# Kernel tuning notes

Hardware: AMD Instinct MI355X
Metric: run time of the kernel (lower is better)

Reference implementation:

```python
import jax, jax.numpy as jnp
import numpy as np

T, B, IN, H, OUT = 512, 1024, 128, 256, 4

def setup_inputs() -> dict:
    key = jax.random.key(0)
    ks = jax.random.split(key, 6)
    return {
        "inp": jax.random.normal(ks[0], (T, B, IN), dtype=jnp.float32),
        "hidden": jnp.zeros((B, H), dtype=jnp.float32),
        "W_i2h": jax.random.normal(ks[1], (H, IN + H), dtype=jnp.float32) * (1.0 / np.sqrt(IN + H)),
        "b_i2h": jax.random.normal(ks[2], (H,), dtype=jnp.float32) * 0.01,
        "W_i2o": jax.random.normal(ks[3], (OUT, IN + H), dtype=jnp.float32) * (1.0 / np.sqrt(IN + H)),
        "b_i2o": jax.random.normal(ks[4], (OUT,), dtype=jnp.float32) * 0.01,
        "actions": jax.random.normal(ks[5], (4, H), dtype=jnp.float32) * 0.01,
    }

def reference(inp, hidden, W_i2h, b_i2h, W_i2o, b_i2o, actions):
    # One RNN step: concat -> two linears -> tanh -> argmax-gated hidden scaling.
    # argmax(softmax(out)) == argmax(out) since softmax is monotone.
    def step(h, x):
        combined = jnp.concatenate([x, h], axis=1)          # [B, IN+H]
        new_h = jnp.tanh(combined @ W_i2h.T + b_i2h)        # [B, H]
        out = combined @ W_i2o.T + b_i2o                    # [B, 4]
        q_idx = jnp.argmax(out, axis=1)                     # [B]
        h_next = new_h * (1.0 + actions[q_idx])             # [B, H]
        return h_next, (out, new_h)

    _, (outs, hs) = jax.lax.scan(step, hidden, inp)
    t, b, o = outs.shape
    # torch.cat(output) concatenates the per-step [B,4] logits along dim 0
    return outs.reshape(t * b, o), hs[0]
```

## Files before the change

kernel.cpp:

```cpp
#include <hip/hip_runtime.h>
#include <hip/hip_bf16.h>


#define TT    512
#define BBAT  1024
#define INDIM 128
#define HDIM  256
#define KDIM  384
#define NB    16
#define HREG  8192
#define XOFF  16384
#define XSLOT 4096

typedef __attribute__((ext_vector_type(8))) __bf16 bf16x8;
typedef __attribute__((ext_vector_type(4))) float  fx4;
typedef __attribute__((ext_vector_type(4))) unsigned int ui4;

__device__ __forceinline__ __bf16 f2bf(float f) {
  unsigned u = __builtin_bit_cast(unsigned, f);
  unsigned short r = (unsigned short)((u + 0x7FFFu + ((u >> 16) & 1u)) >> 16);
  return __builtin_bit_cast(__bf16, r);
}

__device__ __forceinline__ void ldsbar() {
  asm volatile("s_waitcnt lgkmcnt(0)\n\ts_barrier" ::: "memory");
}

__global__ __launch_bounds__(512, 2) void rnn_fused(
    const float* __restrict__ inp,
    const float* __restrict__ hidden,
    const float* __restrict__ Wih,
    const float* __restrict__ bih,
    const float* __restrict__ Wio,
    const float* __restrict__ bio,
    const float* __restrict__ act,
    float* __restrict__ out)
{
  __shared__ __align__(16) char lds[2 * HREG + 4 * XSLOT];

  const int tid  = threadIdx.x;
  const int wave = tid >> 6;
  const int lane = tid & 63;
  const int l15  = lane & 15;
  const int qq   = lane >> 4;
  const int b0   = blockIdx.x * NB;
  const int swz  = l15 & 7;

  float* outs = out;
  float* hs0  = out + (long)TT * BBAT * 4;

  const float C2 = 2.8853900817779268f;

  const int xrow = tid >> 5, xcg = tid & 31;
  fx4 xs[2];
  auto loadx = [&](int t, int s) {
    if (t < TT)
      xs[s] = *(const fx4*)(inp + ((long)t * BBAT + b0 + xrow) * INDIM + xcg * 4);
  };
  const int xwoff = xrow * 256 + (((xcg >> 1) ^ (xrow & 7)) << 4) + (xcg & 1) * 8;
  auto writex = [&](int s, char* dst) {
    union { unsigned long long u; __hip_bfloat162 h2[2]; } pk;
    pk.h2[0] = __float22bfloat162_rn(make_float2(xs[s][0], xs[s][1]));
    pk.h2[1] = __float22bfloat162_rn(make_float2(xs[s][2], xs[s][3]));
    *(unsigned long long*)(dst + xwoff) = pk.u;
  };

  loadx(0, 0);
  {
    const int row = tid >> 5, cg = tid & 31;
    const float* hp = hidden + (long)(b0 + row) * HDIM + cg * 8;
    union { ui4 v; __hip_bfloat162 h2[4]; } pk;
    pk.h2[0] = __float22bfloat162_rn(make_float2(hp[0], hp[1]));
    pk.h2[1] = __float22bfloat162_rn(make_float2(hp[2], hp[3]));
    pk.h2[2] = __float22bfloat162_rn(make_float2(hp[4], hp[5]));
    pk.h2[3] = __float22bfloat162_rn(make_float2(hp[6], hp[7]));
    *(ui4*)(&lds[0] + row * 512 + ((cg ^ (row & 7)) << 4)) = pk.v;
  }
  writex(0, &lds[XOFF + 0 * XSLOT]);
  loadx(1, 1);
  writex(1, &lds[XOFF + 1 * XSLOT]);
  loadx(2, 0);

  bf16x8 Wfr[3][12];
#pragma unroll
  for (int j = 0; j < 3; ++j) {
    const float* wbase = (j < 2) ? (Wih + (long)((wave * 2 + j) * 16 + l15) * KDIM)
                                 : (Wio + (long)(l15 & 3) * KDIM);
#pragma unroll
    for (int kc = 0; kc < 12; ++kc) {
      const float* wp = wbase + kc * 32 + qq * 8;
      bf16x8 f;
#pragma unroll
      for (int i = 0; i < 8; ++i) f[i] = f2bf(wp[i]);
      Wfr[j][kc] = f;
    }
  }

  ui4 abf[4];
#pragma unroll
  for (int qi = 0; qi < 4; ++qi) {
    const fx4 a0 = *(const fx4*)&act[qi * HDIM + (wave * 2 + 0) * 16 + qq * 4];
    const fx4 a1 = *(const fx4*)&act[qi * HDIM + (wave * 2 + 1) * 16 + qq * 4];
    union { ui4 v; __hip_bfloat162 h2[4]; } pk;
    pk.h2[0] = __float22bfloat162_rn(make_float2(a0[0], a0[1]));
    pk.h2[1] = __float22bfloat162_rn(make_float2(a0[2], a0[3]));
    pk.h2[2] = __float22bfloat162_rn(make_float2(a1[0], a1[1]));
    pk.h2[3] = __float22bfloat162_rn(make_float2(a1[2], a1[3]));
    abf[qi] = pk.v;
  }

  fx4 cbz[2];
#pragma unroll
  for (int j = 0; j < 2; ++j)
    cbz[j] = (*(const fx4*)&bih[(wave * 2 + j) * 16 + qq * 4]) * C2;
  const fx4 bo = *(const fx4*)&bio[0];

  const int B0  = (qq ^ (swz & 3)) << 4;
  const int b64 = (swz & 4) << 4;
  const int hE = l15 * 512 + B0 + b64;
  const int hO = l15 * 512 + B0 + 64 - b64;
  const int xE = l15 * 256 + B0 + b64;
  const int xO = l15 * 256 + B0 + 64 - b64;
  int woffH[2];
#pragma unroll
  for (int j = 0; j < 2; ++j)
    woffH[j] = l15 * 512 +
               (((wave * 4 + j * 2 + (qq >> 1)) ^ swz) << 4) + (qq & 1) * 8;

  __syncthreads();

  fx4 acc[2], accL;
  {
    const char* xR = &lds[XOFF];
    bf16x8 xb[4];
    xb[0] = *(const bf16x8*)(xR + xE);
    xb[1] = *(const bf16x8*)(xR + xO);
    xb[2] = *(const bf16x8*)(xR + xE + 128);
    xb[3] = *(const bf16x8*)(xR + xO + 128);
    const fx4 z4 = {0.f, 0.f, 0.f, 0.f};
    accL = z4; acc[0] = z4; acc[1] = z4;
#pragma unroll
    for (int kc = 0; kc < 4; ++kc) {
      accL   = __builtin_amdgcn_mfma_f32_16x16x32_bf16(Wfr[2][kc], xb[kc], accL, 0, 0, 0);
      acc[0] = __builtin_amdgcn_mfma_f32_16x16x32_bf16(Wfr[0][kc], xb[kc], acc[0], 0, 0, 0);
      acc[1] = __builtin_amdgcn_mfma_f32_16x16x32_bf16(Wfr[1][kc], xb[kc], acc[1], 0, 0, 0);
    }
  }

  auto stepf = [&](int t, const int ph) {
    const char* hR = &lds[(ph & 1) * HREG];
    char*       hW = &lds[((ph & 1) ^ 1) * HREG];
    const char* xR = &lds[XOFF + ((ph + 1) & 3) * XSLOT];
    char*       xW = &lds[XOFF + ((ph + 2) & 3) * XSLOT];

    bf16x8 hbA[4], hbB[4];
    hbA[0] = *(const bf16x8*)(hR + hE);
    hbA[1] = *(const bf16x8*)(hR + hO);
    hbA[2] = *(const bf16x8*)(hR + hE + 128);
    hbA[3] = *(const bf16x8*)(hR + hO + 128);
    loadx(t + 3, (ph + 1) & 1);
    hbB[0] = *(const bf16x8*)(hR + hE + 256);
    hbB[1] = *(const bf16x8*)(hR + hO + 256);
    hbB[2] = *(const bf16x8*)(hR + hE + 384);
    hbB[3] = *(const bf16x8*)(hR + hO + 384);

#pragma unroll
    for (int kc = 0; kc < 4; ++kc) {
      accL   = __builtin_amdgcn_mfma_f32_16x16x32_bf16(Wfr[2][kc + 4], hbA[kc], accL, 0, 0, 0);
      acc[0] = __builtin_amdgcn_mfma_f32_16x16x32_bf16(Wfr[0][kc + 4], hbA[kc], acc[0], 0, 0, 0);
      acc[1] = __builtin_amdgcn_mfma_f32_16x16x32_bf16(Wfr[1][kc + 4], hbA[kc], acc[1], 0, 0, 0);
    }
#pragma unroll
    for (int kc = 0; kc < 4; ++kc) {
      accL   = __builtin_amdgcn_mfma_f32_16x16x32_bf16(Wfr[2][kc + 8], hbB[kc], accL, 0, 0, 0);
      acc[0] = __builtin_amdgcn_mfma_f32_16x16x32_bf16(Wfr[0][kc + 8], hbB[kc], acc[0], 0, 0, 0);
      acc[1] = __builtin_amdgcn_mfma_f32_16x16x32_bf16(Wfr[1][kc + 8], hbB[kc], acc[1], 0, 0, 0);
    }

    bf16x8 xb[4];
    if (ph != 3 || t + 1 < TT) {
      xb[0] = *(const bf16x8*)(xR + xE);
      xb[1] = *(const bf16x8*)(xR + xO);
      xb[2] = *(const bf16x8*)(xR + xE + 128);
      xb[3] = *(const bf16x8*)(xR + xO + 128);
    }

    const fx4 lg = accL + bo;
    int qi = 0; float bv = lg[0];
    if (lg[1] > bv) { bv = lg[1]; qi = 1; }
    if (lg[2] > bv) { bv = lg[2]; qi = 2; }
    if (lg[3] > bv) { bv = lg[3]; qi = 3; }
    if (wave == 0 && qq == 0)
      *(fx4*)&outs[((long)t * BBAT + b0 + l15) * 4] = lg;

    const bool s0 = (qi & 1) != 0, s1 = (qi & 2) != 0;
    const ui4 ga = s0 ? abf[1] : abf[0];
    const ui4 gb = s0 ? abf[3] : abf[2];
    const ui4 g  = s1 ? gb : ga;

#pragma unroll
    for (int j = 0; j < 2; ++j) {
      const fx4 z = acc[j] * C2 + cbz[j];
      fx4 th;
#pragma unroll
      for (int r = 0; r < 4; ++r) {
        const float e  = __builtin_amdgcn_exp2f(z[r]);
        const float rc = __builtin_amdgcn_rcpf(e + 1.0f);
        th[r] = fmaf(-2.0f, rc, 1.0f);
      }
      if (ph == 0 && t == 0)
        *(fx4*)&hs0[(long)(b0 + l15) * HDIM + (wave * 2 + j) * 16 + qq * 4] = th;
      const unsigned ug0 = g[j * 2 + 0], ug1 = g[j * 2 + 1];
      const float a0 = __builtin_bit_cast(float, ug0 << 16);
      const float a1 = __builtin_bit_cast(float, ug0 & 0xFFFF0000u);
      const float a2 = __builtin_bit_cast(float, ug1 << 16);
      const float a3 = __builtin_bit_cast(float, ug1 & 0xFFFF0000u);
      fx4 hg;
      hg[0] = fmaf(th[0], a0, th[0]);
      hg[1] = fmaf(th[1], a1, th[1]);
      hg[2] = fmaf(th[2], a2, th[2]);
      hg[3] = fmaf(th[3], a3, th[3]);
      union { unsigned long long u; __hip_bfloat162 h2[2]; } pk;
      pk.h2[0] = __float22bfloat162_rn(make_float2(hg[0], hg[1]));
      pk.h2[1] = __float22bfloat162_rn(make_float2(hg[2], hg[3]));
      *(unsigned long long*)(hW + woffH[j]) = pk.u;
    }

    if (ph != 3 || t + 1 < TT) {
      const fx4 z4 = {0.f, 0.f, 0.f, 0.f};
      accL = z4; acc[0] = z4; acc[1] = z4;
#pragma unroll
      for (int kc = 0; kc < 4; ++kc) {
        accL   = __builtin_amdgcn_mfma_f32_16x16x32_bf16(Wfr[2][kc], xb[kc], accL, 0, 0, 0);
        acc[0] = __builtin_amdgcn_mfma_f32_16x16x32_bf16(Wfr[0][kc], xb[kc], acc[0], 0, 0, 0);
        acc[1] = __builtin_amdgcn_mfma_f32_16x16x32_bf16(Wfr[1][kc], xb[kc], acc[1], 0, 0, 0);
      }
    }

    if (ph < 2 || t + 2 < TT) writex(ph & 1, xW);

    ldsbar();
  };

#pragma unroll 1
  for (int t = 0; t < TT; t += 4) {
    stepf(t,     0);
    stepf(t + 1, 1);
    stepf(t + 2, 2);
    stepf(t + 3, 3);
  }
}

extern "C" void kernel_launch(void* const* d_in, const int* in_sizes, int n_in,
                              void* d_out, int out_size, void* d_ws, size_t ws_size,
                              hipStream_t stream) {
  const float* inp    = (const float*)d_in[0];
  const float* hidden = (const float*)d_in[1];
  const float* Wih    = (const float*)d_in[2];
  const float* bih    = (const float*)d_in[3];
  const float* Wio    = (const float*)d_in[4];
  const float* bio    = (const float*)d_in[5];
  const float* act    = (const float*)d_in[6];
  float* out = (float*)d_out;
  rnn_fused<<<dim3(BBAT / NB), dim3(512), 0, stream>>>(
      inp, hidden, Wih, bih, Wio, bio, act, out);
}
```

Measured before the change: 784.6 us.

## Load x directly into MFMA fragment registers instead of staging through LDS

Removes the LDS staging ring for the input x. Each lane now reads its own MFMA-fragment slice of x from global memory and converts it to bf16 in registers, one step ahead of use. This drops the per-step LDS writes and reads of x and shrinks shared memory to the two h buffers, so the loop unroll goes from 4 to 2 phases. In exchange, all 8 waves load the same x tile redundantly through the cache, the prefetch distance is shorter, and more registers stay live, which under the existing launch bounds could cause spills.

```diff
diff --git a/kernel.cpp b/kernel.cpp
--- a/kernel.cpp
+++ b/kernel.cpp
@@ -9,8 +9,6 @@
 #define KDIM  384
 #define NB    16
 #define HREG  8192
-#define XOFF  16384
-#define XSLOT 4096
 
 typedef __attribute__((ext_vector_type(8))) __bf16 bf16x8;
 typedef __attribute__((ext_vector_type(4))) float  fx4;
@@ -36,7 +34,7 @@
     const float* __restrict__ act,
     float* __restrict__ out)
 {
-  __shared__ __align__(16) char lds[2 * HREG + 4 * XSLOT];
+  __shared__ __align__(16) char lds[2 * HREG];
 
   const int tid  = threadIdx.x;
   const int wave = tid >> 6;
@@ -51,21 +49,30 @@
 
   const float C2 = 2.8853900817779268f;
 
-  const int xrow = tid >> 5, xcg = tid & 31;
-  fx4 xs[2];
-  auto loadx = [&](int t, int s) {
-    if (t < TT)
-      xs[s] = *(const fx4*)(inp + ((long)t * BBAT + b0 + xrow) * INDIM + xcg * 4);
+  const float* xlp = inp + (long)(b0 + l15) * INDIM + qq * 8;
+  fx4 xld[4][2];
+  auto loadxg = [&](int t) {
+    const float* p = xlp + (long)t * (BBAT * INDIM);
+#pragma unroll
+    for (int kc = 0; kc < 4; ++kc) {
+      xld[kc][0] = *(const fx4*)(p + kc * 32);
+      xld[kc][1] = *(const fx4*)(p + kc * 32 + 4);
+    }
   };
-  const int xwoff = xrow * 256 + (((xcg >> 1) ^ (xrow & 7)) << 4) + (xcg & 1) * 8;
-  auto writex = [&](int s, char* dst) {
-    union { unsigned long long u; __hip_bfloat162 h2[2]; } pk;
-    pk.h2[0] = __float22bfloat162_rn(make_float2(xs[s][0], xs[s][1]));
-    pk.h2[1] = __float22bfloat162_rn(make_float2(xs[s][2], xs[s][3]));
-    *(unsigned long long*)(dst + xwoff) = pk.u;
+  auto cvtx = [&](bf16x8* xb) {
+#pragma unroll
+    for (int kc = 0; kc < 4; ++kc) {
+      union { bf16x8 b; __hip_bfloat162 h2[4]; } pk;
+      pk.h2[0] = __float22bfloat162_rn(make_float2(xld[kc][0][0], xld[kc][0][1]));
+      pk.h2[1] = __float22bfloat162_rn(make_float2(xld[kc][0][2], xld[kc][0][3]));
+      pk.h2[2] = __float22bfloat162_rn(make_float2(xld[kc][1][0], xld[kc][1][1]));
+      pk.h2[3] = __float22bfloat162_rn(make_float2(xld[kc][1][2], xld[kc][1][3]));
+      xb[kc] = pk.b;
+    }
   };
 
-  loadx(0, 0);
+  loadxg(0);
+
   {
     const int row = tid >> 5, cg = tid & 31;
     const float* hp = hidden + (long)(b0 + row) * HDIM + cg * 8;
@@ -76,10 +83,6 @@
     pk.h2[3] = __float22bfloat162_rn(make_float2(hp[6], hp[7]));
     *(ui4*)(&lds[0] + row * 512 + ((cg ^ (row & 7)) << 4)) = pk.v;
   }
-  writex(0, &lds[XOFF + 0 * XSLOT]);
-  loadx(1, 1);
-  writex(1, &lds[XOFF + 1 * XSLOT]);
-  loadx(2, 0);
 
   bf16x8 Wfr[3][12];
 #pragma unroll
@@ -119,8 +122,6 @@
   const int b64 = (swz & 4) << 4;
   const int hE = l15 * 512 + B0 + b64;
   const int hO = l15 * 512 + B0 + 64 - b64;
-  const int xE = l15 * 256 + B0 + b64;
-  const int xO = l15 * 256 + B0 + 64 - b64;
   int woffH[2];
 #pragma unroll
   for (int j = 0; j < 2; ++j)
@@ -131,12 +132,8 @@
 
   fx4 acc[2], accL;
   {
-    const char* xR = &lds[XOFF];
     bf16x8 xb[4];
-    xb[0] = *(const bf16x8*)(xR + xE);
-    xb[1] = *(const bf16x8*)(xR + xO);
-    xb[2] = *(const bf16x8*)(xR + xE + 128);
-    xb[3] = *(const bf16x8*)(xR + xO + 128);
+    cvtx(xb);
     const fx4 z4 = {0.f, 0.f, 0.f, 0.f};
     accL = z4; acc[0] = z4; acc[1] = z4;
 #pragma unroll
@@ -146,19 +143,17 @@
       acc[1] = __builtin_amdgcn_mfma_f32_16x16x32_bf16(Wfr[1][kc], xb[kc], acc[1], 0, 0, 0);
     }
   }
+  loadxg(1);
 
   auto stepf = [&](int t, const int ph) {
-    const char* hR = &lds[(ph & 1) * HREG];
-    char*       hW = &lds[((ph & 1) ^ 1) * HREG];
-    const char* xR = &lds[XOFF + ((ph + 1) & 3) * XSLOT];
-    char*       xW = &lds[XOFF + ((ph + 2) & 3) * XSLOT];
+    const char* hR = &lds[ph * HREG];
+    char*       hW = &lds[(ph ^ 1) * HREG];
 
     bf16x8 hbA[4], hbB[4];
     hbA[0] = *(const bf16x8*)(hR + hE);
     hbA[1] = *(const bf16x8*)(hR + hO);
     hbA[2] = *(const bf16x8*)(hR + hE + 128);
     hbA[3] = *(const bf16x8*)(hR + hO + 128);
-    loadx(t + 3, (ph + 1) & 1);
     hbB[0] = *(const bf16x8*)(hR + hE + 256);
     hbB[1] = *(const bf16x8*)(hR + hO + 256);
     hbB[2] = *(const bf16x8*)(hR + hE + 384);
@@ -175,14 +170,6 @@
       accL   = __builtin_amdgcn_mfma_f32_16x16x32_bf16(Wfr[2][kc + 8], hbB[kc], accL, 0, 0, 0);
       acc[0] = __builtin_amdgcn_mfma_f32_16x16x32_bf16(Wfr[0][kc + 8], hbB[kc], acc[0], 0, 0, 0);
       acc[1] = __builtin_amdgcn_mfma_f32_16x16x32_bf16(Wfr[1][kc + 8], hbB[kc], acc[1], 0, 0, 0);
-    }
-
-    bf16x8 xb[4];
-    if (ph != 3 || t + 1 < TT) {
-      xb[0] = *(const bf16x8*)(xR + xE);
-      xb[1] = *(const bf16x8*)(xR + xO);
-      xb[2] = *(const bf16x8*)(xR + xE + 128);
-      xb[3] = *(const bf16x8*)(xR + xO + 128);
     }
 
     const fx4 lg = accL + bo;
@@ -226,7 +213,9 @@
       *(unsigned long long*)(hW + woffH[j]) = pk.u;
     }
 
-    if (ph != 3 || t + 1 < TT) {
+    if (t + 1 < TT) {
+      bf16x8 xb[4];
+      cvtx(xb);
       const fx4 z4 = {0.f, 0.f, 0.f, 0.f};
       accL = z4; acc[0] = z4; acc[1] = z4;
 #pragma unroll
@@ -235,19 +224,16 @@
         acc[0] = __builtin_amdgcn_mfma_f32_16x16x32_bf16(Wfr[0][kc], xb[kc], acc[0], 0, 0, 0);
         acc[1] = __builtin_amdgcn_mfma_f32_16x16x32_bf16(Wfr[1][kc], xb[kc], acc[1], 0, 0, 0);
       }
-    }
-
-    if (ph < 2 || t + 2 < TT) writex(ph & 1, xW);
+      if (t + 2 < TT) loadxg(t + 2);
+    }
 
     ldsbar();
   };
 
 #pragma unroll 1
-  for (int t = 0; t < TT; t += 4) {
+  for (int t = 0; t < TT; t += 2) {
     stepf(t,     0);
     stepf(t + 1, 1);
-    stepf(t + 2, 2);
-    stepf(t + 3, 3);
   }
 }
 
```

New measurement: 1.180 ms. +50.4%, slower.
